# Optimization experiments

Measured on AMD Instinct MI355X. Metric: run time of the kernel, lower is better.

The kernel has to match this reference:

```python
import jax, jax.numpy as jnp
import numpy as np

GRID_RES_SAMPLE = 0.08  # config.grid_resolution_sample
VOXEL_SIZE = 0.04       # scene voxel size encoded in transforms


def setup_inputs() -> dict:
    key = jax.random.key(0)
    ks = jax.random.split(key, 4)
    B, X = 4, 96
    G = 192            # == ceil(X * GRID_RES_SAMPLE / VOXEL_SIZE), matches dynamic size_voxel_grid
    N = 500_000        # sparse occupied voxels per scene
    NUM_ADD = 5000     # static stand-in for occ_grids.sum()+100 mask augmentations
    # scene voxel-grid transform: scale VOXEL_SIZE, translate -5m (same structure per scene)
    T = np.eye(4, dtype=np.float32)
    T[0, 0] = T[1, 1] = T[2, 2] = VOXEL_SIZE
    T[:3, 3] = -5.0
    transforms = np.tile(T, (B, 1, 1)).astype(np.float32)
    transforms_inv = np.stack([np.linalg.inv(t) for t in transforms]).astype(np.float32)
    # per-batch regular coordinate grids with random world offsets in [0,1)m
    offs = np.asarray(jax.random.uniform(ks[0], (B, 3), dtype=jnp.float32))
    ax = np.arange(X, dtype=np.float32) * GRID_RES_SAMPLE
    gx, gy, gz = np.meshgrid(ax, ax, ax, indexing='ij')
    base = np.stack([gx, gy, gz], axis=0)  # [3,X,X,X]
    coords = (base[None] + offs[:, :, None, None, None]).astype(np.float32)
    sparse = jax.random.randint(ks[1], (B, N, 3), 0, 400, dtype=jnp.int32)
    rand_idx = jax.random.randint(ks[2], (3, NUM_ADD), 0, X, dtype=jnp.int32)
    conv_w = jnp.ones((1, 1, 5, 5, 5), jnp.float32)  # Conv3d(1,1,5) all-ones, no bias
    return {
        'coordinate_grids': jnp.asarray(coords),
        'transforms': jnp.asarray(transforms),
        'transforms_inv': jnp.asarray(transforms_inv),
        'sparse_encoding': sparse,
        'conv_w': conv_w,
        'rand_idx': rand_idx,
        'grid_size': G,
    }


def reference(coordinate_grids, transforms, transforms_inv, sparse_encoding, conv_w, rand_idx, grid_size):
    B, C, X, Y, Z = coordinate_grids.shape
    flat = coordinate_grids.reshape(B, 3, -1)
    min_loc = flat.min(-1)   # [B,3]
    max_loc = flat.max(-1)   # [B,3]
    max_size_grid = (max_loc + GRID_RES_SAMPLE - min_loc).max(0)  # [3]
    min_homo = jnp.concatenate([min_loc, jnp.ones((B, 1), flat.dtype)], axis=1)
    min_voxel_idx = jnp.floor(jnp.einsum('bij,bj->bi', transforms_inv, min_homo)[:, :3])
    min_voxel_idx = jnp.maximum(min_voxel_idx, 0.0)  # [B,3]
    size_vox = jnp.ceil(jnp.einsum('bij,j->bi', transforms_inv[:, :3, :3], max_size_grid).max(0))  # [3], == grid_size
    # shift sparse indices into the local window and filter out-of-range ones
    se = sparse_encoding.astype(jnp.float32) - min_voxel_idx[:, None, :]   # [B,N,3]
    valid = ((se >= 0) & (se < size_vox)).all(-1)                          # [B,N]
    sei = jnp.clip(se.astype(jnp.int32), 0, grid_size - 1)
    occ = jnp.zeros((B, grid_size, grid_size, grid_size), jnp.float32)
    b_idx = jnp.broadcast_to(jnp.arange(B)[:, None], valid.shape)
    occ = occ.at[b_idx, sei[..., 0], sei[..., 1], sei[..., 2]].max(valid.astype(jnp.float32))
    # world position of voxel (0,0,0) of the local window and window extent
    min_homo_idx = jnp.concatenate([min_voxel_idx, jnp.ones((B, 1), flat.dtype)], axis=1)
    pos_base = jnp.einsum('bij,bj->bi', transforms, min_homo_idx)[:, :3]   # [B,3]
    extent = jnp.einsum('bij,j->bi', transforms[:, :3, :3], size_vox)      # [B,3]
    voxel_size = extent / size_vox                                          # [B,3]
    # trilinear interpolation of dense occ grid at the coordinate grid (voxel-center convention)
    p = (coordinate_grids - pos_base[:, :, None, None, None]) / voxel_size[:, :, None, None, None] - 0.5
    p0 = jnp.floor(p)
    f = p - p0                       # [B,3,X,Y,Z]
    p0 = p0.astype(jnp.int32)
    bb = jnp.arange(B)[:, None, None, None]
    out = jnp.zeros((B, X, Y, Z), jnp.float32)
    for dx in (0, 1):
        for dy in (0, 1):
            for dz in (0, 1):
                ix = jnp.clip(p0[:, 0] + dx, 0, grid_size - 1)
                iy = jnp.clip(p0[:, 1] + dy, 0, grid_size - 1)
                iz = jnp.clip(p0[:, 2] + dz, 0, grid_size - 1)
                w = ((f[:, 0] if dx else 1 - f[:, 0]) *
                     (f[:, 1] if dy else 1 - f[:, 1]) *
                     (f[:, 2] if dz else 1 - f[:, 2]))
                out = out + w * occ[bb, ix, iy, iz]
    occ_grids = out[:, None]  # [B,1,X,Y,Z]
    # 5x5x5 all-ones conv mask
    conv = jax.lax.conv_general_dilated(
        occ_grids, conv_w, window_strides=(1, 1, 1),
        padding=[(2, 2), (2, 2), (2, 2)],
        dimension_numbers=('NCDHW', 'OIDHW', 'NCDHW'))
    mask = conv > 0
    # random-index mask augmentation (num_voxels_to_add fixed statically)
    num_add = rand_idx.shape[1]
    badd = jnp.arange(num_add) % B
    mask = mask.at[badd, 0, rand_idx[0], rand_idx[1], rand_idx[2]].set(True)
    return occ_grids.astype(bool), mask
```

## Files before the change

kernel.cpp:

```cpp
#include <hip/hip_runtime.h>
#include <math.h>

#define GS   192
#define XS   96
#define XS3  (XS*XS*XS)
#define GRS  0.08f

#define PI_OFF     256
#define PF_OFF     (256 + 1152*4)
#define OCC_OFF    16384
#define OCC_WORDS  (4*GS*GS*(GS/32))
#define OUTB_WORDS (4*XS*XS*(XS/32))
#define RAND_OFF   (OCC_OFF + OCC_WORDS*4)
#define OUT_OFF    (RAND_OFF + OUTB_WORDS*4)

__device__ __forceinline__ int clampi(int v, int lo, int hi) {
    return v < lo ? lo : (v > hi ? hi : v);
}

__global__ void k_scalars(const float* __restrict__ coords,
                          const float* __restrict__ T,
                          const float* __restrict__ Tinv,
                          float* ws,
                          const int* __restrict__ rand_idx,
                          unsigned* __restrict__ randb,
                          int B, int nadd) {
    __shared__ int imn[12], imx[12];
    __shared__ float SS[64];
    int t = threadIdx.x;
    for (int idx = t; idx < nadd; idx += 256) {
        int b = idx % B;
        int r0 = rand_idx[idx], r1 = rand_idx[nadd + idx], r2 = rand_idx[2*nadd + idx];
        int e = ((b*XS + r0)*XS + r1)*XS + r2;
        atomicOr(&randb[e >> 5], 1u << (e & 31));
    }
    if (t < 12) { imn[t] = 0x7F800000; imx[t] = 0; }
    __syncthreads();
    int tot = B * 3 * XS;
    for (int e = t; e < tot; e += 256) {
        int b = e / (3 * XS); int c = (e / XS) % 3; int i = e % XS;
        size_t off = (size_t)(b*3 + c) * XS3
                   + (c == 0 ? (size_t)i * XS * XS : (c == 1 ? (size_t)i * XS : (size_t)i));
        int v = __float_as_int(coords[off]);
        atomicMin(&imn[b*3 + c], v);
        atomicMax(&imx[b*3 + c], v);
    }
    __syncthreads();
    if (t == 0) {
        float mnl[12], mxl[12];
        for (int k = 0; k < 12; k++) { mnl[k] = __int_as_float(imn[k]); mxl[k] = __int_as_float(imx[k]); }
        float msg[3];
        for (int c = 0; c < 3; c++) {
            float m = -__builtin_inff();
            for (int b = 0; b < B; b++) {
                float v = __fadd_rn(mxl[b*3 + c], GRS);
                v = __fsub_rn(v, mnl[b*3 + c]);
                m = fmaxf(m, v);
            }
            msg[c] = m;
        }
        for (int b = 0; b < B; b++)
            for (int i = 0; i < 3; i++) {
                const float* R = Tinv + b*16 + i*4;
                float v = __fmul_rn(R[0], mnl[b*3 + 0]);
                v = __fadd_rn(v, __fmul_rn(R[1], mnl[b*3 + 1]));
                v = __fadd_rn(v, __fmul_rn(R[2], mnl[b*3 + 2]));
                v = __fadd_rn(v, R[3]);
                SS[24 + b*3 + i] = fmaxf(floorf(v), 0.0f);
            }
        for (int i = 0; i < 3; i++) {
            float m = -__builtin_inff();
            for (int b = 0; b < B; b++) {
                const float* R = Tinv + b*16 + i*4;
                float v = __fmul_rn(R[0], msg[0]);
                v = __fadd_rn(v, __fmul_rn(R[1], msg[1]));
                v = __fadd_rn(v, __fmul_rn(R[2], msg[2]));
                m = fmaxf(m, v);
            }
            SS[36 + i] = ceilf(m);
        }
        for (int b = 0; b < B; b++)
            for (int i = 0; i < 3; i++) {
                const float* R = T + b*16 + i*4;
                float v = __fmul_rn(R[0], SS[24 + b*3 + 0]);
                v = __fadd_rn(v, __fmul_rn(R[1], SS[24 + b*3 + 1]));
                v = __fadd_rn(v, __fmul_rn(R[2], SS[24 + b*3 + 2]));
                v = __fadd_rn(v, R[3]);
                SS[40 + b*3 + i] = v;
            }
        for (int b = 0; b < B; b++)
            for (int i = 0; i < 3; i++) {
                const float* R = T + b*16 + i*4;
                float v = __fmul_rn(R[0], SS[36 + 0]);
                v = __fadd_rn(v, __fmul_rn(R[1], SS[36 + 1]));
                v = __fadd_rn(v, __fmul_rn(R[2], SS[36 + 2]));
                SS[52 + b*3 + i] = v / SS[36 + i];
            }
        for (int k = 24; k < 64; k++) ws[k] = SS[k];
    }
    __syncthreads();
    int* PI = (int*)((char*)ws + PI_OFF);
    float* PF = (float*)((char*)ws + PF_OFF);
    for (int e = t; e < tot; e += 256) {
        int b = e / (3 * XS); int c = (e / XS) % 3; int i = e % XS;
        size_t off = (size_t)(b*3 + c) * XS3
                   + (c == 0 ? (size_t)i * XS * XS : (c == 1 ? (size_t)i * XS : (size_t)i));
        float v = coords[off];
        float p = (v - SS[40 + b*3 + c]) / SS[52 + b*3 + c] - 0.5f;
        float p0 = floorf(p);
        PI[e] = (int)p0;
        PF[e] = p - p0;
    }
}

__global__ void k_scatter(const int* __restrict__ sparse, const float* __restrict__ ws,
                          unsigned* __restrict__ occ, int N, int total) {
    int t = blockIdx.x * blockDim.x + threadIdx.x;
    if (t >= total) return;
    int b = t / N;
    const float* S = ws;
    int s0 = sparse[(size_t)t*3 + 0];
    int s1 = sparse[(size_t)t*3 + 1];
    int s2 = sparse[(size_t)t*3 + 2];
    float e0 = (float)s0 - S[24 + b*3 + 0];
    float e1 = (float)s1 - S[24 + b*3 + 1];
    float e2 = (float)s2 - S[24 + b*3 + 2];
    if (e0 >= 0.f && e0 < S[36+0] && e1 >= 0.f && e1 < S[36+1] && e2 >= 0.f && e2 < S[36+2]) {
        int x = clampi((int)e0, 0, GS-1);
        int y = clampi((int)e1, 0, GS-1);
        int z = clampi((int)e2, 0, GS-1);
        atomicOr(&occ[(((size_t)b*GS + x)*GS + y)*(GS/32) + (z >> 5)], 1u << (z & 31));
    }
}

__global__ __launch_bounds__(256) void k_interp(const float* __restrict__ ws,
                                                const unsigned* __restrict__ occ,
                                                int* __restrict__ out0,
                                                unsigned* __restrict__ outb,
                                                int total) {
    int gid = blockIdx.x * 256 + threadIdx.x;
    if (gid >= total) return;
    int z = gid % XS;
    int r1 = gid / XS;
    int y = r1 % XS;
    int r2 = r1 / XS;
    int x = r2 % XS;
    int b = r2 / XS;
    const int* PI = (const int*)((const char*)ws + PI_OFF);
    const float* PF = (const float*)((const char*)ws + PF_OFF);
    int ix = PI[(b*3 + 0)*XS + x]; float fx = PF[(b*3 + 0)*XS + x];
    int iy = PI[(b*3 + 1)*XS + y]; float fy = PF[(b*3 + 1)*XS + y];
    int iz = PI[(b*3 + 2)*XS + z]; float fz = PF[(b*3 + 2)*XS + z];
    int x0 = clampi(ix,   0, GS-1), x1 = clampi(ix+1, 0, GS-1);
    int y0 = clampi(iy,   0, GS-1), y1 = clampi(iy+1, 0, GS-1);
    int z0 = clampi(iz,   0, GS-1), z1 = clampi(iz+1, 0, GS-1);
    float wx0 = 1.f - fx, wx1 = fx, wy0 = 1.f - fy, wy1 = fy, wz0 = 1.f - fz, wz1 = fz;
    const unsigned* r00 = occ + (((size_t)b*GS + x0)*GS + y0)*(GS/32);
    const unsigned* r01 = occ + (((size_t)b*GS + x0)*GS + y1)*(GS/32);
    const unsigned* r10 = occ + (((size_t)b*GS + x1)*GS + y0)*(GS/32);
    const unsigned* r11 = occ + (((size_t)b*GS + x1)*GS + y1)*(GS/32);
    float w00 = wx0*wy0, w01 = wx0*wy1, w10 = wx1*wy0, w11 = wx1*wy1;
    float s = 0.f;
    s += w00*wz0*(float)((r00[z0>>5] >> (z0&31)) & 1u);
    s += w00*wz1*(float)((r00[z1>>5] >> (z1&31)) & 1u);
    s += w01*wz0*(float)((r01[z0>>5] >> (z0&31)) & 1u);
    s += w01*wz1*(float)((r01[z1>>5] >> (z1&31)) & 1u);
    s += w10*wz0*(float)((r10[z0>>5] >> (z0&31)) & 1u);
    s += w10*wz1*(float)((r10[z1>>5] >> (z1&31)) & 1u);
    s += w11*wz0*(float)((r11[z0>>5] >> (z0&31)) & 1u);
    s += w11*wz1*(float)((r11[z1>>5] >> (z1&31)) & 1u);
    bool nz = (s != 0.f);
    out0[gid] = nz ? 1 : 0;
    unsigned long long m = __ballot(nz);
    int lane = threadIdx.x & 63;
    if (lane == 0)  outb[gid >> 5] = (unsigned)m;
    if (lane == 32) outb[gid >> 5] = (unsigned)(m >> 32);
}

__global__ __launch_bounds__(256) void k_dilate_expand(const unsigned* __restrict__ outb,
                                                       const unsigned* __restrict__ randb,
                                                       int* __restrict__ out1) {
    int t = blockIdx.x * 256 + threadIdx.x;
    int w = t % 3;
    int r1 = t / 3;
    int j = r1 % XS;
    int r2 = r1 / XS;
    int i = r2 % XS;
    int b = r2 / XS;
    unsigned accP = 0, accC = 0, accN = 0;
    for (int di = -2; di <= 2; di++) {
        int ii = i + di; if (ii < 0 || ii >= XS) continue;
        for (int dj = -2; dj <= 2; dj++) {
            int jj = j + dj; if (jj < 0 || jj >= XS) continue;
            const unsigned* row = outb + ((size_t)(b*XS + ii)*XS + jj)*3;
            accC |= row[w];
            if (w > 0) accP |= row[w-1];
            if (w < 2) accN |= row[w+1];
        }
    }
    unsigned d = accC
               | (accC << 1) | (accP >> 31)
               | (accC << 2) | (accP >> 30)
               | (accC >> 1) | (accN << 31)
               | (accC >> 2) | (accN << 30);
    d |= randb[t];
    __shared__ unsigned lds[256];
    lds[threadIdx.x] = d;
    __syncthreads();
    size_t base = (size_t)blockIdx.x * 8192;
    #pragma unroll
    for (int k = 0; k < 32; k++) {
        int e = k * 256 + threadIdx.x;
        out1[base + e] = (int)((lds[e >> 5] >> (e & 31)) & 1u);
    }
}

extern "C" void kernel_launch(void* const* d_in, const int* in_sizes, int n_in,
                              void* d_out, int out_size, void* d_ws, size_t ws_size,
                              hipStream_t stream) {
    const float* coords = (const float*)d_in[0];
    const float* T      = (const float*)d_in[1];
    const float* Tinv   = (const float*)d_in[2];
    const int*   sparse = (const int*)d_in[3];
    const int*   rand_i = (const int*)d_in[5];
    int* out = (int*)d_out;

    int B = in_sizes[1] / 16;
    int N = in_sizes[3] / (B * 3);
    int nadd = in_sizes[5] / 3;

    float*    ws    = (float*)d_ws;
    unsigned* occ   = (unsigned*)((char*)d_ws + OCC_OFF);
    unsigned* randb = (unsigned*)((char*)d_ws + RAND_OFF);
    unsigned* outb  = (unsigned*)((char*)d_ws + OUT_OFF);
    size_t half = (size_t)B * XS3;

    hipMemsetAsync((char*)d_ws + OCC_OFF, 0, (size_t)(OCC_WORDS + OUTB_WORDS) * 4, stream);

    k_scalars<<<1, 256, 0, stream>>>(coords, T, Tinv, ws, rand_i, randb, B, nadd);
    int totalPts = B * N;
    k_scatter<<<(totalPts + 255) / 256, 256, 0, stream>>>(sparse, ws, occ, N, totalPts);
    int total = B * XS3;
    k_interp<<<(total + 255) / 256, 256, 0, stream>>>(ws, occ, out, outb, total);
    int totalW = B * XS * XS * 3;
    k_dilate_expand<<<totalW / 256, 256, 0, stream>>>(outb, randb, out + half);
}
```

Before: 161.1 us.

## Fuse memset, scalar, scatter, interp and dilation stages into one cooperative kernel

Replaces the memset and four separate launches with a single persistent cooperative kernel of 1024 blocks that moves between stages with grid-wide syncs. Block 0 computes the scalar transforms while the other blocks zero the occupancy and random-mask bitmaps. Each block then caches the per-axis interpolation tables in LDS, and the dilated mask is staged in the occupancy region, which is free by then, before the final expansion. This removes launch gaps and the separate memset, but adds grid-sync costs and relies on every block being co-resident.

Measured after the change: 628.3 us. 290% more time.

```diff
diff --git a/kernel.cpp b/kernel.cpp
--- a/kernel.cpp
+++ b/kernel.cpp
@@ -1,5 +1,8 @@
 #include <hip/hip_runtime.h>
+#include <hip/hip_cooperative_groups.h>
 #include <math.h>
+
+namespace cg = cooperative_groups;
 
 #define GS   192
 #define XS   96
@@ -18,201 +21,215 @@
     return v < lo ? lo : (v > hi ? hi : v);
 }
 
-__global__ void k_scalars(const float* __restrict__ coords,
-                          const float* __restrict__ T,
-                          const float* __restrict__ Tinv,
-                          float* ws,
-                          const int* __restrict__ rand_idx,
-                          unsigned* __restrict__ randb,
-                          int B, int nadd) {
-    __shared__ int imn[12], imx[12];
-    __shared__ float SS[64];
-    int t = threadIdx.x;
-    for (int idx = t; idx < nadd; idx += 256) {
-        int b = idx % B;
-        int r0 = rand_idx[idx], r1 = rand_idx[nadd + idx], r2 = rand_idx[2*nadd + idx];
+__global__ __launch_bounds__(256, 4) void k_fused(
+    const float* __restrict__ coords, const float* __restrict__ T,
+    const float* __restrict__ Tinv, const int* __restrict__ sparse,
+    const int* __restrict__ rand_idx, float* ws, int* out,
+    int B, int N, int nadd)
+{
+    cg::grid_group grid = cg::this_grid();
+    const int tid  = threadIdx.x;
+    const int gtid = blockIdx.x * 256 + tid;
+    const int gsz  = gridDim.x * 256;
+
+    unsigned* occ   = (unsigned*)((char*)ws + OCC_OFF);
+    unsigned* randb = (unsigned*)((char*)ws + RAND_OFF);
+    unsigned* outb  = (unsigned*)((char*)ws + OUT_OFF);
+    unsigned* outb2 = occ;
+    int* out0 = out;
+    int* out1 = out + (size_t)B * XS3;
+    const int total  = B * XS3;
+    const int totalW = B * XS * XS * 3;
+
+    __shared__ int   sPI[1152];
+    __shared__ float sPF[1152];
+    __shared__ float sS[64];
+
+    if (blockIdx.x == 0) {
+        __shared__ int imn[12], imx[12];
+        if (tid < 12) { imn[tid] = 0x7F800000; imx[tid] = 0; }
+        __syncthreads();
+        int tot = B * 3 * XS;
+        for (int e = tid; e < tot; e += 256) {
+            int b = e / (3 * XS); int c = (e / XS) % 3; int i = e % XS;
+            size_t off = (size_t)(b*3 + c) * XS3
+                       + (c == 0 ? (size_t)i * XS * XS : (c == 1 ? (size_t)i * XS : (size_t)i));
+            int v = __float_as_int(coords[off]);
+            atomicMin(&imn[b*3 + c], v);
+            atomicMax(&imx[b*3 + c], v);
+        }
+        __syncthreads();
+        if (tid == 0) {
+            float mnl[12], mxl[12];
+            for (int k = 0; k < 12; k++) { mnl[k] = __int_as_float(imn[k]); mxl[k] = __int_as_float(imx[k]); }
+            float msg[3];
+            for (int c = 0; c < 3; c++) {
+                float m = -__builtin_inff();
+                for (int b = 0; b < B; b++) {
+                    float v = __fadd_rn(mxl[b*3 + c], GRS);
+                    v = __fsub_rn(v, mnl[b*3 + c]);
+                    m = fmaxf(m, v);
+                }
+                msg[c] = m;
+            }
+            for (int b = 0; b < B; b++)
+                for (int i = 0; i < 3; i++) {
+                    const float* R = Tinv + b*16 + i*4;
+                    float v = __fmul_rn(R[0], mnl[b*3 + 0]);
+                    v = __fadd_rn(v, __fmul_rn(R[1], mnl[b*3 + 1]));
+                    v = __fadd_rn(v, __fmul_rn(R[2], mnl[b*3 + 2]));
+                    v = __fadd_rn(v, R[3]);
+                    sS[24 + b*3 + i] = fmaxf(floorf(v), 0.0f);
+                }
+            for (int i = 0; i < 3; i++) {
+                float m = -__builtin_inff();
+                for (int b = 0; b < B; b++) {
+                    const float* R = Tinv + b*16 + i*4;
+                    float v = __fmul_rn(R[0], msg[0]);
+                    v = __fadd_rn(v, __fmul_rn(R[1], msg[1]));
+                    v = __fadd_rn(v, __fmul_rn(R[2], msg[2]));
+                    m = fmaxf(m, v);
+                }
+                sS[36 + i] = ceilf(m);
+            }
+            for (int b = 0; b < B; b++)
+                for (int i = 0; i < 3; i++) {
+                    const float* R = T + b*16 + i*4;
+                    float v = __fmul_rn(R[0], sS[24 + b*3 + 0]);
+                    v = __fadd_rn(v, __fmul_rn(R[1], sS[24 + b*3 + 1]));
+                    v = __fadd_rn(v, __fmul_rn(R[2], sS[24 + b*3 + 2]));
+                    v = __fadd_rn(v, R[3]);
+                    sS[40 + b*3 + i] = v;
+                }
+            for (int b = 0; b < B; b++)
+                for (int i = 0; i < 3; i++) {
+                    const float* R = T + b*16 + i*4;
+                    float v = __fmul_rn(R[0], sS[36 + 0]);
+                    v = __fadd_rn(v, __fmul_rn(R[1], sS[36 + 1]));
+                    v = __fadd_rn(v, __fmul_rn(R[2], sS[36 + 2]));
+                    sS[52 + b*3 + i] = v / sS[36 + i];
+                }
+            for (int k = 24; k < 64; k++) ws[k] = sS[k];
+        }
+        __syncthreads();
+        int* PI = (int*)((char*)ws + PI_OFF);
+        float* PF = (float*)((char*)ws + PF_OFF);
+        for (int e = tid; e < tot; e += 256) {
+            int b = e / (3 * XS); int c = (e / XS) % 3; int i = e % XS;
+            size_t off = (size_t)(b*3 + c) * XS3
+                       + (c == 0 ? (size_t)i * XS * XS : (c == 1 ? (size_t)i * XS : (size_t)i));
+            float v = coords[off];
+            float p = (v - sS[40 + b*3 + c]) / sS[52 + b*3 + c] - 0.5f;
+            float p0 = floorf(p);
+            PI[e] = (int)p0;
+            PF[e] = p - p0;
+        }
+        __threadfence();
+    } else {
+        const int zw = OCC_WORDS + OUTB_WORDS;
+        for (int w = (blockIdx.x - 1) * 256 + tid; w < zw; w += (gridDim.x - 1) * 256)
+            occ[w] = 0u;
+    }
+    grid.sync();
+
+    if (tid < 64) sS[tid] = ws[tid];
+    {
+        const int* PI = (const int*)((const char*)ws + PI_OFF);
+        const float* PF = (const float*)((const char*)ws + PF_OFF);
+        for (int e = tid; e < 1152; e += 256) { sPI[e] = PI[e]; sPF[e] = PF[e]; }
+    }
+    __syncthreads();
+
+    for (int t = gtid; t < B * N; t += gsz) {
+        int b = t / N;
+        int s0 = sparse[(size_t)t*3 + 0];
+        int s1 = sparse[(size_t)t*3 + 1];
+        int s2 = sparse[(size_t)t*3 + 2];
+        float e0 = (float)s0 - sS[24 + b*3 + 0];
+        float e1 = (float)s1 - sS[24 + b*3 + 1];
+        float e2 = (float)s2 - sS[24 + b*3 + 2];
+        if (e0 >= 0.f && e0 < sS[36+0] && e1 >= 0.f && e1 < sS[36+1] && e2 >= 0.f && e2 < sS[36+2]) {
+            int x = clampi((int)e0, 0, GS-1);
+            int y = clampi((int)e1, 0, GS-1);
+            int z = clampi((int)e2, 0, GS-1);
+            atomicOr(&occ[(((size_t)b*GS + x)*GS + y)*(GS/32) + (z >> 5)], 1u << (z & 31));
+        }
+    }
+    for (int i = gtid; i < nadd; i += gsz) {
+        int b = i % B;
+        int r0 = rand_idx[i], r1 = rand_idx[nadd + i], r2 = rand_idx[2*nadd + i];
         int e = ((b*XS + r0)*XS + r1)*XS + r2;
         atomicOr(&randb[e >> 5], 1u << (e & 31));
     }
-    if (t < 12) { imn[t] = 0x7F800000; imx[t] = 0; }
-    __syncthreads();
-    int tot = B * 3 * XS;
-    for (int e = t; e < tot; e += 256) {
-        int b = e / (3 * XS); int c = (e / XS) % 3; int i = e % XS;
-        size_t off = (size_t)(b*3 + c) * XS3
-                   + (c == 0 ? (size_t)i * XS * XS : (c == 1 ? (size_t)i * XS : (size_t)i));
-        int v = __float_as_int(coords[off]);
-        atomicMin(&imn[b*3 + c], v);
-        atomicMax(&imx[b*3 + c], v);
-    }
-    __syncthreads();
-    if (t == 0) {
-        float mnl[12], mxl[12];
-        for (int k = 0; k < 12; k++) { mnl[k] = __int_as_float(imn[k]); mxl[k] = __int_as_float(imx[k]); }
-        float msg[3];
-        for (int c = 0; c < 3; c++) {
-            float m = -__builtin_inff();
-            for (int b = 0; b < B; b++) {
-                float v = __fadd_rn(mxl[b*3 + c], GRS);
-                v = __fsub_rn(v, mnl[b*3 + c]);
-                m = fmaxf(m, v);
+    grid.sync();
+
+    for (int gid = gtid; gid < total; gid += gsz) {
+        int z  = gid % XS;
+        int r1 = gid / XS;
+        int y  = r1 % XS;
+        int r2 = r1 / XS;
+        int x  = r2 % XS;
+        int b  = r2 / XS;
+        int ix = sPI[(b*3 + 0)*XS + x]; float fx = sPF[(b*3 + 0)*XS + x];
+        int iy = sPI[(b*3 + 1)*XS + y]; float fy = sPF[(b*3 + 1)*XS + y];
+        int iz = sPI[(b*3 + 2)*XS + z]; float fz = sPF[(b*3 + 2)*XS + z];
+        int x0 = clampi(ix,   0, GS-1), x1 = clampi(ix+1, 0, GS-1);
+        int y0 = clampi(iy,   0, GS-1), y1 = clampi(iy+1, 0, GS-1);
+        int z0 = clampi(iz,   0, GS-1), z1 = clampi(iz+1, 0, GS-1);
+        float wx0 = 1.f - fx, wx1 = fx, wy0 = 1.f - fy, wy1 = fy, wz0 = 1.f - fz, wz1 = fz;
+        const unsigned* r00 = occ + (((size_t)b*GS + x0)*GS + y0)*(GS/32);
+        const unsigned* r01 = occ + (((size_t)b*GS + x0)*GS + y1)*(GS/32);
+        const unsigned* r10 = occ + (((size_t)b*GS + x1)*GS + y0)*(GS/32);
+        const unsigned* r11 = occ + (((size_t)b*GS + x1)*GS + y1)*(GS/32);
+        float w00 = wx0*wy0, w01 = wx0*wy1, w10 = wx1*wy0, w11 = wx1*wy1;
+        float s = 0.f;
+        s += w00*wz0*(float)((r00[z0>>5] >> (z0&31)) & 1u);
+        s += w00*wz1*(float)((r00[z1>>5] >> (z1&31)) & 1u);
+        s += w01*wz0*(float)((r01[z0>>5] >> (z0&31)) & 1u);
+        s += w01*wz1*(float)((r01[z1>>5] >> (z1&31)) & 1u);
+        s += w10*wz0*(float)((r10[z0>>5] >> (z0&31)) & 1u);
+        s += w10*wz1*(float)((r10[z1>>5] >> (z1&31)) & 1u);
+        s += w11*wz0*(float)((r11[z0>>5] >> (z0&31)) & 1u);
+        s += w11*wz1*(float)((r11[z1>>5] >> (z1&31)) & 1u);
+        bool nz = (s != 0.f);
+        out0[gid] = nz ? 1 : 0;
+        unsigned long long m = __ballot(nz);
+        int lane = tid & 63;
+        if (lane == 0)  outb[gid >> 5] = (unsigned)m;
+        if (lane == 32) outb[gid >> 5] = (unsigned)(m >> 32);
+    }
+    grid.sync();
+
+    for (int t = gtid; t < totalW; t += gsz) {
+        int w  = t % 3;
+        int r1 = t / 3;
+        int j  = r1 % XS;
+        int r2 = r1 / XS;
+        int i  = r2 % XS;
+        int b  = r2 / XS;
+        unsigned accP = 0, accC = 0, accN = 0;
+        for (int di = -2; di <= 2; di++) {
+            int ii = i + di; if (ii < 0 || ii >= XS) continue;
+            for (int dj = -2; dj <= 2; dj++) {
+                int jj = j + dj; if (jj < 0 || jj >= XS) continue;
+                const unsigned* row = outb + ((size_t)(b*XS + ii)*XS + jj)*3;
+                accC |= row[w];
+                if (w > 0) accP |= row[w-1];
+                if (w < 2) accN |= row[w+1];
             }
-            msg[c] = m;
-        }
-        for (int b = 0; b < B; b++)
-            for (int i = 0; i < 3; i++) {
-                const float* R = Tinv + b*16 + i*4;
-                float v = __fmul_rn(R[0], mnl[b*3 + 0]);
-                v = __fadd_rn(v, __fmul_rn(R[1], mnl[b*3 + 1]));
-                v = __fadd_rn(v, __fmul_rn(R[2], mnl[b*3 + 2]));
-                v = __fadd_rn(v, R[3]);
-                SS[24 + b*3 + i] = fmaxf(floorf(v), 0.0f);
-            }
-        for (int i = 0; i < 3; i++) {
-            float m = -__builtin_inff();
-            for (int b = 0; b < B; b++) {
-                const float* R = Tinv + b*16 + i*4;
-                float v = __fmul_rn(R[0], msg[0]);
-                v = __fadd_rn(v, __fmul_rn(R[1], msg[1]));
-                v = __fadd_rn(v, __fmul_rn(R[2], msg[2]));
-                m = fmaxf(m, v);
-            }
-            SS[36 + i] = ceilf(m);
-        }
-        for (int b = 0; b < B; b++)
-            for (int i = 0; i < 3; i++) {
-                const float* R = T + b*16 + i*4;
-                float v = __fmul_rn(R[0], SS[24 + b*3 + 0]);
-                v = __fadd_rn(v, __fmul_rn(R[1], SS[24 + b*3 + 1]));
-                v = __fadd_rn(v, __fmul_rn(R[2], SS[24 + b*3 + 2]));
-                v = __fadd_rn(v, R[3]);
-                SS[40 + b*3 + i] = v;
-            }
-        for (int b = 0; b < B; b++)
-            for (int i = 0; i < 3; i++) {
-                const float* R = T + b*16 + i*4;
-                float v = __fmul_rn(R[0], SS[36 + 0]);
-                v = __fadd_rn(v, __fmul_rn(R[1], SS[36 + 1]));
-                v = __fadd_rn(v, __fmul_rn(R[2], SS[36 + 2]));
-                SS[52 + b*3 + i] = v / SS[36 + i];
-            }
-        for (int k = 24; k < 64; k++) ws[k] = SS[k];
-    }
-    __syncthreads();
-    int* PI = (int*)((char*)ws + PI_OFF);
-    float* PF = (float*)((char*)ws + PF_OFF);
-    for (int e = t; e < tot; e += 256) {
-        int b = e / (3 * XS); int c = (e / XS) % 3; int i = e % XS;
-        size_t off = (size_t)(b*3 + c) * XS3
-                   + (c == 0 ? (size_t)i * XS * XS : (c == 1 ? (size_t)i * XS : (size_t)i));
-        float v = coords[off];
-        float p = (v - SS[40 + b*3 + c]) / SS[52 + b*3 + c] - 0.5f;
-        float p0 = floorf(p);
-        PI[e] = (int)p0;
-        PF[e] = p - p0;
-    }
-}
-
-__global__ void k_scatter(const int* __restrict__ sparse, const float* __restrict__ ws,
-                          unsigned* __restrict__ occ, int N, int total) {
-    int t = blockIdx.x * blockDim.x + threadIdx.x;
-    if (t >= total) return;
-    int b = t / N;
-    const float* S = ws;
-    int s0 = sparse[(size_t)t*3 + 0];
-    int s1 = sparse[(size_t)t*3 + 1];
-    int s2 = sparse[(size_t)t*3 + 2];
-    float e0 = (float)s0 - S[24 + b*3 + 0];
-    float e1 = (float)s1 - S[24 + b*3 + 1];
-    float e2 = (float)s2 - S[24 + b*3 + 2];
-    if (e0 >= 0.f && e0 < S[36+0] && e1 >= 0.f && e1 < S[36+1] && e2 >= 0.f && e2 < S[36+2]) {
-        int x = clampi((int)e0, 0, GS-1);
-        int y = clampi((int)e1, 0, GS-1);
-        int z = clampi((int)e2, 0, GS-1);
-        atomicOr(&occ[(((size_t)b*GS + x)*GS + y)*(GS/32) + (z >> 5)], 1u << (z & 31));
-    }
-}
-
-__global__ __launch_bounds__(256) void k_interp(const float* __restrict__ ws,
-                                                const unsigned* __restrict__ occ,
-                                                int* __restrict__ out0,
-                                                unsigned* __restrict__ outb,
-                                                int total) {
-    int gid = blockIdx.x * 256 + threadIdx.x;
-    if (gid >= total) return;
-    int z = gid % XS;
-    int r1 = gid / XS;
-    int y = r1 % XS;
-    int r2 = r1 / XS;
-    int x = r2 % XS;
-    int b = r2 / XS;
-    const int* PI = (const int*)((const char*)ws + PI_OFF);
-    const float* PF = (const float*)((const char*)ws + PF_OFF);
-    int ix = PI[(b*3 + 0)*XS + x]; float fx = PF[(b*3 + 0)*XS + x];
-    int iy = PI[(b*3 + 1)*XS + y]; float fy = PF[(b*3 + 1)*XS + y];
-    int iz = PI[(b*3 + 2)*XS + z]; float fz = PF[(b*3 + 2)*XS + z];
-    int x0 = clampi(ix,   0, GS-1), x1 = clampi(ix+1, 0, GS-1);
-    int y0 = clampi(iy,   0, GS-1), y1 = clampi(iy+1, 0, GS-1);
-    int z0 = clampi(iz,   0, GS-1), z1 = clampi(iz+1, 0, GS-1);
-    float wx0 = 1.f - fx, wx1 = fx, wy0 = 1.f - fy, wy1 = fy, wz0 = 1.f - fz, wz1 = fz;
-    const unsigned* r00 = occ + (((size_t)b*GS + x0)*GS + y0)*(GS/32);
-    const unsigned* r01 = occ + (((size_t)b*GS + x0)*GS + y1)*(GS/32);
-    const unsigned* r10 = occ + (((size_t)b*GS + x1)*GS + y0)*(GS/32);
-    const unsigned* r11 = occ + (((size_t)b*GS + x1)*GS + y1)*(GS/32);
-    float w00 = wx0*wy0, w01 = wx0*wy1, w10 = wx1*wy0, w11 = wx1*wy1;
-    float s = 0.f;
-    s += w00*wz0*(float)((r00[z0>>5] >> (z0&31)) & 1u);
-    s += w00*wz1*(float)((r00[z1>>5] >> (z1&31)) & 1u);
-    s += w01*wz0*(float)((r01[z0>>5] >> (z0&31)) & 1u);
-    s += w01*wz1*(float)((r01[z1>>5] >> (z1&31)) & 1u);
-    s += w10*wz0*(float)((r10[z0>>5] >> (z0&31)) & 1u);
-    s += w10*wz1*(float)((r10[z1>>5] >> (z1&31)) & 1u);
-    s += w11*wz0*(float)((r11[z0>>5] >> (z0&31)) & 1u);
-    s += w11*wz1*(float)((r11[z1>>5] >> (z1&31)) & 1u);
-    bool nz = (s != 0.f);
-    out0[gid] = nz ? 1 : 0;
-    unsigned long long m = __ballot(nz);
-    int lane = threadIdx.x & 63;
-    if (lane == 0)  outb[gid >> 5] = (unsigned)m;
-    if (lane == 32) outb[gid >> 5] = (unsigned)(m >> 32);
-}
-
-__global__ __launch_bounds__(256) void k_dilate_expand(const unsigned* __restrict__ outb,
-                                                       const unsigned* __restrict__ randb,
-                                                       int* __restrict__ out1) {
-    int t = blockIdx.x * 256 + threadIdx.x;
-    int w = t % 3;
-    int r1 = t / 3;
-    int j = r1 % XS;
-    int r2 = r1 / XS;
-    int i = r2 % XS;
-    int b = r2 / XS;
-    unsigned accP = 0, accC = 0, accN = 0;
-    for (int di = -2; di <= 2; di++) {
-        int ii = i + di; if (ii < 0 || ii >= XS) continue;
-        for (int dj = -2; dj <= 2; dj++) {
-            int jj = j + dj; if (jj < 0 || jj >= XS) continue;
-            const unsigned* row = outb + ((size_t)(b*XS + ii)*XS + jj)*3;
-            accC |= row[w];
-            if (w > 0) accP |= row[w-1];
-            if (w < 2) accN |= row[w+1];
-        }
-    }
-    unsigned d = accC
-               | (accC << 1) | (accP >> 31)
-               | (accC << 2) | (accP >> 30)
-               | (accC >> 1) | (accN << 31)
-               | (accC >> 2) | (accN << 30);
-    d |= randb[t];
-    __shared__ unsigned lds[256];
-    lds[threadIdx.x] = d;
-    __syncthreads();
-    size_t base = (size_t)blockIdx.x * 8192;
-    #pragma unroll
-    for (int k = 0; k < 32; k++) {
-        int e = k * 256 + threadIdx.x;
-        out1[base + e] = (int)((lds[e >> 5] >> (e & 31)) & 1u);
-    }
+        }
+        unsigned d = accC
+                   | (accC << 1) | (accP >> 31)
+                   | (accC << 2) | (accP >> 30)
+                   | (accC >> 1) | (accN << 31)
+                   | (accC >> 2) | (accN << 30);
+        d |= randb[t];
+        outb2[t] = d;
+    }
+    grid.sync();
+
+    for (int gid = gtid; gid < total; gid += gsz)
+        out1[gid] = (int)((outb2[gid >> 5] >> (gid & 31)) & 1u);
 }
 
 extern "C" void kernel_launch(void* const* d_in, const int* in_sizes, int n_in,
@@ -228,20 +245,11 @@
     int B = in_sizes[1] / 16;
     int N = in_sizes[3] / (B * 3);
     int nadd = in_sizes[5] / 3;
-
-    float*    ws    = (float*)d_ws;
-    unsigned* occ   = (unsigned*)((char*)d_ws + OCC_OFF);
-    unsigned* randb = (unsigned*)((char*)d_ws + RAND_OFF);
-    unsigned* outb  = (unsigned*)((char*)d_ws + OUT_OFF);
-    size_t half = (size_t)B * XS3;
-
-    hipMemsetAsync((char*)d_ws + OCC_OFF, 0, (size_t)(OCC_WORDS + OUTB_WORDS) * 4, stream);
-
-    k_scalars<<<1, 256, 0, stream>>>(coords, T, Tinv, ws, rand_i, randb, B, nadd);
-    int totalPts = B * N;
-    k_scatter<<<(totalPts + 255) / 256, 256, 0, stream>>>(sparse, ws, occ, N, totalPts);
-    int total = B * XS3;
-    k_interp<<<(total + 255) / 256, 256, 0, stream>>>(ws, occ, out, outb, total);
-    int totalW = B * XS * XS * 3;
-    k_dilate_expand<<<totalW / 256, 256, 0, stream>>>(outb, randb, out + half);
+    float* ws = (float*)d_ws;
+
+    void* args[] = { (void*)&coords, (void*)&T, (void*)&Tinv, (void*)&sparse,
+                     (void*)&rand_i, (void*)&ws, (void*)&out,
+                     (void*)&B, (void*)&N, (void*)&nadd };
+    hipLaunchCooperativeKernel((void*)k_fused, dim3(1024), dim3(256),
+                               args, 0, stream);
 }
```
